# Kernel tuning notes

Hardware: AMD Instinct MI355X
Metric: run time of the kernel (lower is better)

The kernel has to match this reference:

```python
import jax, jax.numpy as jnp
import numpy as np

B, S, D, H, F = 2, 2048, 3072, 32, 8192
DH = D // H  # 96
EPS = 1e-5


def setup_inputs() -> dict:
    key = jax.random.key(0)
    ks = jax.random.split(key, 16)
    sd = 0.02
    inp = {
        "hidden_states": jax.random.normal(ks[0], (B, S, D), jnp.float32),
        "ln1_g": jnp.ones((D,), jnp.float32),
        "ln1_b": jnp.zeros((D,), jnp.float32),
        "Wq": jax.random.normal(ks[1], (D, H, DH), jnp.float32) * sd,
        "bq": jnp.zeros((H, DH), jnp.float32),
        "Wk": jax.random.normal(ks[2], (D, H, DH), jnp.float32) * sd,
        "bk": jnp.zeros((H, DH), jnp.float32),
        "Wv": jax.random.normal(ks[3], (D, H, DH), jnp.float32) * sd,
        "bv": jnp.zeros((H, DH), jnp.float32),
        "Wo": jax.random.normal(ks[4], (H, DH, D), jnp.float32) * sd,
        "bo": jnp.zeros((D,), jnp.float32),
        "ln2_g": jnp.ones((D,), jnp.float32),
        "ln2_b": jnp.zeros((D,), jnp.float32),
        "W1": jax.random.normal(ks[5], (D, F), jnp.float32) * sd,
        "b1": jnp.zeros((F,), jnp.float32),
        "W2": jax.random.normal(ks[6], (F, D), jnp.float32) * sd,
        "b2": jnp.zeros((D,), jnp.float32),
    }
    return inp


def _layernorm(x, g, b):
    m = jnp.mean(x, axis=-1, keepdims=True)
    v = jnp.mean(jnp.square(x - m), axis=-1, keepdims=True)
    return (x - m) * jax.lax.rsqrt(v + EPS) * g + b


def reference(hidden_states, ln1_g, ln1_b, Wq, bq, Wk, bk, Wv, bv, Wo, bo,
              ln2_g, ln2_b, W1, b1, W2, b2):
    # --- LN + self-attention + residual ---
    h = _layernorm(hidden_states, ln1_g, ln1_b)  # [B,S,D]
    q = jnp.einsum('bsd,dhk->bshk', h, Wq) + bq  # [B,S,H,DH]
    k = jnp.einsum('bsd,dhk->bshk', h, Wk) + bk
    v = jnp.einsum('bsd,dhk->bshk', h, Wv) + bv
    scale = 1.0 / np.sqrt(DH).astype(np.float32)
    scores = jnp.einsum('bshk,bthk->bhst', q, k) * scale  # [B,H,S,S]
    attn = jax.nn.softmax(scores, axis=-1)
    ctx = jnp.einsum('bhst,bthk->bshk', attn, v)  # [B,S,H,DH]
    attn_out = jnp.einsum('bshk,hkd->bsd', ctx, Wo) + bo
    h1 = hidden_states + attn_out
    # --- LN + MLP + residual ---
    h2 = _layernorm(h1, ln2_g, ln2_b)
    mlp = jax.nn.gelu(h2 @ W1 + b1, approximate=False) @ W2 + b2
    return h1 + mlp
```

## Files before the change

### kernel.cpp

```cpp
#include <hip/hip_runtime.h>
#include <math.h>

#define DEV __device__ __forceinline__

typedef __attribute__((ext_vector_type(8))) __bf16 bfrag;
typedef __attribute__((ext_vector_type(4))) float f4;
typedef __attribute__((ext_vector_type(8))) unsigned short u16x8;
typedef __attribute__((ext_vector_type(4))) unsigned short u16x4;

DEV unsigned short f2bf(float f) {
  unsigned u = __float_as_uint(f);
  u += 0x7fff + ((u >> 16) & 1);
  return (unsigned short)(u >> 16);
}

DEV void gload_lds16(const void* g, void* l) {
  __builtin_amdgcn_global_load_lds((const __attribute__((address_space(1))) void*)g,
                                   (__attribute__((address_space(3))) void*)l, 16, 0, 0);
}

template<int EPI, int OUTBF, int BIASROW>
__global__ __launch_bounds__(256, 2)
void gemm_bt(const unsigned short* __restrict__ A,
             const unsigned short* __restrict__ Bt,
             const float* __restrict__ bias,
             const float* __restrict__ res,
             void* __restrict__ outp,
             int M, int N, int K, int gm, int cm, int cn)
{
  __shared__ unsigned short As[2][128 * 32];
  __shared__ unsigned short Bs[2][128 * 32];
  const int tid = threadIdx.x;
  const int lane = tid & 63;
  const int wid = tid >> 6;
  const int wr = wid >> 1, wc = wid & 1;
  const int l15 = lane & 15, lg = lane >> 4;

  const int xcd = blockIdx.x & 7, bidx = blockIdx.x >> 3;
  const int cgm = gm / cm;
  const int tm = (xcd % cgm) * cm + bidx % cm;
  const int tn = (xcd / cgm) * cn + bidx / cm;
  const long tM = (long)tm * 128;
  const long tN = (long)tn * 128;

  const int c0 = tid, c1 = tid + 256;
  const int r0 = c0 >> 2, k0 = (c0 & 3) * 8;
  const int r1 = c1 >> 2, k1 = (c1 & 3) * 8;

  const unsigned short* A0 = A + (tM + r0) * (long)K + k0;
  const unsigned short* A1 = A + (tM + r1) * (long)K + k1;
  const unsigned short* B0 = Bt + (tN + r0) * (long)K + k0;
  const unsigned short* B1 = Bt + (tN + r1) * (long)K + k1;

  auto stage = [&](int kt, int buf) {
    const long ko = (long)kt * 32;
    gload_lds16(A0 + ko, &As[buf][c0 * 8]);
    gload_lds16(A1 + ko, &As[buf][c1 * 8]);
    gload_lds16(B0 + ko, &Bs[buf][c0 * 8]);
    gload_lds16(B1 + ko, &Bs[buf][c1 * 8]);
  };

  stage(0, 0);
  f4 acc[4][4] = {};
  const int nk = K >> 5;
  int cur = 0;
  __syncthreads();
  for (int kt = 0; kt < nk; ++kt) {
    if (kt + 1 < nk) stage(kt + 1, cur ^ 1);
    bfrag aF[4], bF[4];
#pragma unroll
    for (int m = 0; m < 4; ++m)
      aF[m] = *(const bfrag*)&As[cur][(wr * 64 + m * 16 + l15) * 32 + lg * 8];
#pragma unroll
    for (int n = 0; n < 4; ++n)
      bF[n] = *(const bfrag*)&Bs[cur][(wc * 64 + n * 16 + l15) * 32 + lg * 8];
#pragma unroll
    for (int m = 0; m < 4; ++m)
#pragma unroll
      for (int n = 0; n < 4; ++n)
        acc[m][n] = __builtin_amdgcn_mfma_f32_16x16x32_bf16(aF[m], bF[n], acc[m][n], 0, 0, 0);
    __syncthreads();
    cur ^= 1;
  }

#pragma unroll
  for (int m = 0; m < 4; ++m) {
#pragma unroll
    for (int n = 0; n < 4; ++n) {
      const long col = tN + wc * 64 + n * 16 + l15;
      const float bcol = BIASROW ? 0.f : bias[col];
#pragma unroll
      for (int e = 0; e < 4; ++e) {
        const long row = tM + wr * 64 + m * 16 + lg * 4 + e;
        float v = acc[m][n][e] + (BIASROW ? bias[row] : bcol);
        if constexpr (EPI == 1) v = 0.5f * v * (1.0f + erff(v * 0.70710678118654752f));
        if constexpr (EPI == 2) v += res[row * N + col];
        if constexpr (OUTBF) ((unsigned short*)outp)[row * N + col] = f2bf(v);
        else                 ((float*)outp)[row * N + col] = v;
      }
    }
  }
}

template<int EPI, int OUTBF, int BIASROW>
__global__ __launch_bounds__(512, 2)
void gemm256(const unsigned short* __restrict__ A,
             const unsigned short* __restrict__ Bt,
             const float* __restrict__ bias,
             const float* __restrict__ res,
             void* __restrict__ outp,
             int M, int N, int K, int gm, int cm, int cn)
{
  __shared__ unsigned short As[2][256 * 64];
  __shared__ unsigned short Bs[2][256 * 64];

  const int tid = threadIdx.x;
  const int lane = tid & 63;
  const int wid = tid >> 6;
  const int wm = wid >> 2, wn = wid & 3;
  const int l15 = lane & 15, lg = lane >> 4;

  const int xcd = blockIdx.x & 7, bidx = blockIdx.x >> 3;
  const int cgm = gm / cm;
  const int tm = (xcd % cgm) * cm + bidx % cm;
  const int tn = (xcd / cgm) * cn + bidx / cm;
  const long tM = (long)tm * 256, tN = (long)tn * 256;

  const int srow = tid >> 3;
  const int lslot = (tid & 7) ^ (srow & 7);
  const unsigned short* aSrc = A + (tM + srow) * (long)K + lslot * 8;
  const unsigned short* bSrc = Bt + (tN + srow) * (long)K + lslot * 8;
  const int NT = K >> 6;

  auto stA = [&](int t, int j) {
    gload_lds16(aSrc + (long)t * 64 + (long)j * 64 * K, &As[t & 1][j * 4096 + tid * 8]);
  };
  auto stB = [&](int t, int j) {
    gload_lds16(bSrc + (long)t * 64 + (long)j * 64 * K, &Bs[t & 1][j * 4096 + tid * 8]);
  };

#pragma unroll
  for (int j = 0; j < 4; ++j) stA(0, j);
#pragma unroll
  for (int j = 0; j < 4; ++j) stB(0, j);
  stA(1, 0); stA(1, 2);
#pragma unroll
  for (int j = 0; j < 4; ++j) stB(1, j);
  asm volatile("s_waitcnt vmcnt(6)" ::: "memory");
  __builtin_amdgcn_s_barrier();

  const int aRow = (wm * 128 + l15) * 64;
  const int bRow = (wn * 64 + l15) * 64;
  const int sx = l15 & 7;
  const int sl0 = ((0 + lg) ^ sx) * 8;
  const int sl1 = ((4 + lg) ^ sx) * 8;

  bfrag aL[4][2], aH[4][2], b01[2][2], b23[2][2];
  f4 acc[8][4] = {};

  int cur = 0;
  for (int t = 0; t < NT; ++t, cur ^= 1) {
    const unsigned short* Ac = As[cur];
    const unsigned short* Bc = Bs[cur];
    const bool s1 = (t + 1 < NT);
    const bool s2 = (t + 2 < NT);

#pragma unroll
    for (int m = 0; m < 4; ++m) {
      aL[m][0] = *(const bfrag*)&Ac[aRow + m * 1024 + sl0];
      aL[m][1] = *(const bfrag*)&Ac[aRow + m * 1024 + sl1];
    }
#pragma unroll
    for (int n = 0; n < 2; ++n) {
      b01[n][0] = *(const bfrag*)&Bc[bRow + n * 1024 + sl0];
      b01[n][1] = *(const bfrag*)&Bc[bRow + n * 1024 + sl1];
    }
#pragma unroll
    for (int n = 0; n < 2; ++n) {
      b23[n][0] = *(const bfrag*)&Bc[bRow + (n + 2) * 1024 + sl0];
      b23[n][1] = *(const bfrag*)&Bc[bRow + (n + 2) * 1024 + sl1];
    }
    if (s1) { stA(t + 1, 1); stA(t + 1, 3); }
    __builtin_amdgcn_s_barrier();
    __builtin_amdgcn_s_setprio(1);
#pragma unroll
    for (int m = 0; m < 4; ++m)
#pragma unroll
      for (int n = 0; n < 2; ++n) {
        acc[m][n] = __builtin_amdgcn_mfma_f32_16x16x32_bf16(aL[m][0], b01[n][0], acc[m][n], 0, 0, 0);
        acc[m][n] = __builtin_amdgcn_mfma_f32_16x16x32_bf16(aL[m][1], b01[n][1], acc[m][n], 0, 0, 0);
      }
    __builtin_amdgcn_s_setprio(0);
    __builtin_amdgcn_s_barrier();

#pragma unroll
    for (int m = 0; m < 4; ++m) {
      aH[m][0] = *(const bfrag*)&Ac[aRow + 4096 + m * 1024 + sl0];
      aH[m][1] = *(const bfrag*)&Ac[aRow + 4096 + m * 1024 + sl1];
    }
    if (s2) { stA(t + 2, 0); stA(t + 2, 2); }
    __builtin_amdgcn_s_barrier();
    __builtin_amdgcn_s_setprio(1);
#pragma unroll
    for (int m = 0; m < 4; ++m)
#pragma unroll
      for (int n = 0; n < 2; ++n) {
        acc[m][2 + n] = __builtin_amdgcn_mfma_f32_16x16x32_bf16(aL[m][0], b23[n][0], acc[m][2 + n], 0, 0, 0);
        acc[m][2 + n] = __builtin_amdgcn_mfma_f32_16x16x32_bf16(aL[m][1], b23[n][1], acc[m][2 + n], 0, 0, 0);
      }
    __builtin_amdgcn_s_setprio(0);
    __builtin_amdgcn_s_barrier();

    if (s2) { stB(t + 2, 0); stB(t + 2, 1); }
    __builtin_amdgcn_s_barrier();
    __builtin_amdgcn_s_setprio(1);
#pragma unroll
    for (int m = 0; m < 4; ++m)
#pragma unroll
      for (int n = 0; n < 2; ++n) {
        acc[4 + m][2 + n] = __builtin_amdgcn_mfma_f32_16x16x32_bf16(aH[m][0], b23[n][0], acc[4 + m][2 + n], 0, 0, 0);
        acc[4 + m][2 + n] = __builtin_amdgcn_mfma_f32_16x16x32_bf16(aH[m][1], b23[n][1], acc[4 + m][2 + n], 0, 0, 0);
      }
    __builtin_amdgcn_s_setprio(0);
    __builtin_amdgcn_s_barrier();

    if (s2) { stB(t + 2, 2); stB(t + 2, 3); }
    __builtin_amdgcn_s_setprio(1);
#pragma unroll
    for (int m = 0; m < 4; ++m)
#pragma unroll
      for (int n = 0; n < 2; ++n) {
        acc[4 + m][n] = __builtin_amdgcn_mfma_f32_16x16x32_bf16(aH[m][0], b01[n][0], acc[4 + m][n], 0, 0, 0);
        acc[4 + m][n] = __builtin_amdgcn_mfma_f32_16x16x32_bf16(aH[m][1], b01[n][1], acc[4 + m][n], 0, 0, 0);
      }
    __builtin_amdgcn_s_setprio(0);
    if (s2)      asm volatile("s_waitcnt vmcnt(6)" ::: "memory");
    else if (s1) asm volatile("s_waitcnt vmcnt(0)" ::: "memory");
    __builtin_amdgcn_s_barrier();
  }

#pragma unroll
  for (int m = 0; m < 8; ++m) {
    const long row0 = tM + wm * 128 + m * 16 + lg * 4;
#pragma unroll
    for (int n = 0; n < 4; ++n) {
      const long col = tN + wn * 64 + n * 16 + l15;
      const float bc = BIASROW ? 0.f : bias[col];
#pragma unroll
      for (int e = 0; e < 4; ++e) {
        const long row = row0 + e;
        float v = acc[m][n][e] + (BIASROW ? bias[row] : bc);
        if constexpr (EPI == 1) v = 0.5f * v * (1.0f + erff(v * 0.70710678118654752f));
        if constexpr (EPI == 2) v += res[row * N + col];
        if constexpr (OUTBF) ((unsigned short*)outp)[row * N + col] = f2bf(v);
        else                 ((float*)outp)[row * N + col] = v;
      }
    }
  }
}

__global__ __launch_bounds__(256)
void ln_bf16(const float* __restrict__ x, const float* __restrict__ g,
             const float* __restrict__ b, unsigned short* __restrict__ out)
{
  __shared__ float red[4];
  const int tid = threadIdx.x;
  const long row = blockIdx.x;
  const float* xr = x + row * 3072;
  float4 v[3];
  float s = 0.f;
#pragma unroll
  for (int i = 0; i < 3; ++i) {
    v[i] = *(const float4*)&xr[i * 1024 + tid * 4];
    s += v[i].x + v[i].y + v[i].z + v[i].w;
  }
#pragma unroll
  for (int o = 32; o > 0; o >>= 1) s += __shfl_xor(s, o);
  if ((tid & 63) == 0) red[tid >> 6] = s;
  __syncthreads();
  s = red[0] + red[1] + red[2] + red[3];
  const float mean = s * (1.f / 3072.f);
  float vs = 0.f;
#pragma unroll
  for (int i = 0; i < 3; ++i) {
    const float dx = v[i].x - mean, dy = v[i].y - mean;
    const float dz = v[i].z - mean, dw = v[i].w - mean;
    vs += dx * dx + dy * dy + dz * dz + dw * dw;
  }
#pragma unroll
  for (int o = 32; o > 0; o >>= 1) vs += __shfl_xor(vs, o);
  __syncthreads();
  if ((tid & 63) == 0) red[tid >> 6] = vs;
  __syncthreads();
  vs = red[0] + red[1] + red[2] + red[3];
  const float rstd = rsqrtf(vs * (1.f / 3072.f) + 1e-5f);
#pragma unroll
  for (int i = 0; i < 3; ++i) {
    const int idx = i * 1024 + tid * 4;
    const float* vp = (const float*)&v[i];
    u16x4 o4;
#pragma unroll
    for (int c = 0; c < 4; ++c)
      o4[c] = f2bf((vp[c] - mean) * rstd * g[idx + c] + b[idx + c]);
    *(u16x4*)&out[row * 3072 + idx] = o4;
  }
}

__global__ __launch_bounds__(256)
void prep_weights(const float* __restrict__ Wq, const float* __restrict__ Wk,
                  const float* __restrict__ Wv, const float* __restrict__ Wo,
                  const float* __restrict__ W1, const float* __restrict__ W2,
                  const float* __restrict__ bq, const float* __restrict__ bk,
                  unsigned short* __restrict__ WqkT, unsigned short* __restrict__ WvT,
                  unsigned short* __restrict__ WoT, unsigned short* __restrict__ W1T,
                  unsigned short* __restrict__ W2T, float* __restrict__ bqk)
{
  __shared__ float tile[32][33];
  int bid = blockIdx.x;
  if (bid < 24) {
    const int i = bid * 256 + threadIdx.x;
    bqk[i] = (i < 3072) ? bq[i] : bk[i - 3072];
    return;
  }
  bid -= 24;
  const float* in; unsigned short* out; int R, C, nbx;
  if (bid < 9216)        { in = Wq; out = WqkT;                R = 3072; C = 3072; nbx = 96; }
  else if (bid < 18432)  { in = Wk; out = WqkT + 3072 * 3072;  R = 3072; C = 3072; nbx = 96; bid -= 9216; }
  else if (bid < 27648)  { in = Wv; out = WvT;                 R = 3072; C = 3072; nbx = 96; bid -= 18432; }
  else if (bid < 36864)  { in = Wo; out = WoT;                 R = 3072; C = 3072; nbx = 96; bid -= 27648; }
  else if (bid < 61440)  { in = W1; out = W1T;                 R = 3072; C = 8192; nbx = 256; bid -= 36864; }
  else                   { in = W2; out = W2T;                 R = 8192; C = 3072; nbx = 96; bid -= 61440; }
  const int bx = bid % nbx, by = bid / nbx;
  const int tx = threadIdx.x & 31, ty = threadIdx.x >> 5;
  const long r0 = (long)by * 32, cc0 = (long)bx * 32;
#pragma unroll
  for (int i = 0; i < 4; ++i)
    tile[ty + 8 * i][tx] = in[(r0 + ty + 8 * i) * C + cc0 + tx];
  __syncthreads();
#pragma unroll
  for (int i = 0; i < 4; ++i)
    out[(cc0 + ty + 8 * i) * R + r0 + tx] = f2bf(tile[tx][ty + 8 * i]);
}

__global__ __launch_bounds__(256, 4)
void attn_fwd(const unsigned short* __restrict__ qk,
              const unsigned short* __restrict__ vT,
              unsigned short* __restrict__ ctx)
{
  __shared__ unsigned short Ks[64 * 104];
  __shared__ unsigned short Vt[96 * 72];
  __shared__ unsigned short Ps[4 * 16 * 72];
  const int tid = threadIdx.x;
  const int lane = tid & 63;
  const int w = tid >> 6;
  const int l15 = lane & 15, lg = lane >> 4;
  const int bid = (blockIdx.x & 7) * 256 + (blockIdx.x >> 3);
  const int qb = bid & 31;
  const int h = (bid >> 5) & 31;
  const int b = bid >> 10;
  const long qkbase = ((long)b * 2048) * 6144 + h * 96;
  const long obase  = ((long)b * 2048) * 3072 + h * 96;
  const long vbase  = (long)(h * 96) * 4096 + (long)b * 2048;
  const int qbase = qb * 64;

  bfrag qf[3];
#pragma unroll
  for (int ks = 0; ks < 3; ++ks)
    qf[ks] = *(const bfrag*)&qk[qkbase + (long)(qbase + w * 16 + l15) * 6144 + ks * 32 + lg * 8];

  const int kr0 = tid / 12,         kk0 = (tid % 12) * 8;
  const int kr1 = (tid + 256) / 12, kk1 = ((tid + 256) % 12) * 8;
  const int kr2 = (tid + 512) / 12, kk2 = ((tid + 512) % 12) * 8;
  const unsigned short* kg = qk + qkbase + 3072;
  const int vd0 = tid >> 3,           vk0 = (tid & 7) * 8;
  const int vd1 = (tid + 256) >> 3,   vk1 = ((tid + 256) & 7) * 8;
  const int vd2 = (tid + 512) >> 3,   vk2 = ((tid + 512) & 7) * 8;
  const unsigned short* vg = vT + vbase;

  u16x8 kA = *(const u16x8*)&kg[(long)kr0 * 6144 + kk0];
  u16x8 kB = *(const u16x8*)&kg[(long)kr1 * 6144 + kk1];
  u16x8 kC = *(const u16x8*)&kg[(long)kr2 * 6144 + kk2];
  u16x8 vA = *(const u16x8*)&vg[(long)vd0 * 4096 + vk0];
  u16x8 vB = *(const u16x8*)&vg[(long)vd1 * 4096 + vk1];
  u16x8 vC = *(const u16x8*)&vg[(long)vd2 * 4096 + vk2];

  float m_run = -1e30f, l_run = 0.f;
  f4 O[6] = {};
  const float sc = 0.1020620726f * 1.4426950409f;

  for (int t = 0; t < 32; ++t) {
    *(u16x8*)&Ks[kr0 * 104 + kk0] = kA;
    *(u16x8*)&Ks[kr1 * 104 + kk1] = kB;
    *(u16x8*)&Ks[kr2 * 104 + kk2] = kC;
    *(u16x8*)&Vt[vd0 * 72 + vk0] = vA;
    *(u16x8*)&Vt[vd1 * 72 + vk1] = vB;
    *(u16x8*)&Vt[vd2 * 72 + vk2] = vC;
    __syncthreads();
    if (t + 1 < 32) {
      const long ko = (long)(t + 1) * 64 * 6144;
      const long vo = (long)(t + 1) * 64;
      kA = *(const u16x8*)&kg[ko + (long)kr0 * 6144 + kk0];
      kB = *(const u16x8*)&kg[ko + (long)kr1 * 6144 + kk1];
      kC = *(const u16x8*)&kg[ko + (long)kr2 * 6144 + kk2];
      vA = *(const u16x8*)&vg[vo + (long)vd0 * 4096 + vk0];
      vB = *(const u16x8*)&vg[vo + (long)vd1 * 4096 + vk1];
      vC = *(const u16x8*)&vg[vo + (long)vd2 * 4096 + vk2];
    }

    f4 sf[4];
#pragma unroll
    for (int mb = 0; mb < 4; ++mb) {
      f4 z = {0.f, 0.f, 0.f, 0.f};
      sf[mb] = z;
#pragma unroll
      for (int ks = 0; ks < 3; ++ks) {
        bfrag kf = *(const bfrag*)&Ks[(mb * 16 + l15) * 104 + ks * 32 + lg * 8];
        sf[mb] = __builtin_amdgcn_mfma_f32_16x16x32_bf16(kf, qf[ks], sf[mb], 0, 0, 0);
      }
    }
    float p[16];
    float tmax = -1e30f;
#pragma unroll
    for (int mb = 0; mb < 4; ++mb)
#pragma unroll
      for (int e = 0; e < 4; ++e) {
        const float sv = sf[mb][e] * sc;
        p[mb * 4 + e] = sv;
        tmax = fmaxf(tmax, sv);
      }
    tmax = fmaxf(tmax, __shfl_xor(tmax, 16));
    tmax = fmaxf(tmax, __shfl_xor(tmax, 32));
    const float mnew = fmaxf(m_run, tmax);
    const float alpha = exp2f(m_run - mnew);
    float psum = 0.f;
#pragma unroll
    for (int i = 0; i < 16; ++i) {
      p[i] = exp2f(p[i] - mnew);
      psum += p[i];
    }
    psum += __shfl_xor(psum, 16);
    psum += __shfl_xor(psum, 32);
    l_run = l_run * alpha + psum;
    m_run = mnew;
#pragma unroll
    for (int mb = 0; mb < 4; ++mb) {
      u16x4 pw;
#pragma unroll
      for (int e = 0; e < 4; ++e) pw[e] = f2bf(p[mb * 4 + e]);
      *(u16x4*)&Ps[w * 1152 + l15 * 72 + mb * 16 + lg * 4] = pw;
    }
    float aE[4];
#pragma unroll
    for (int e = 0; e < 4; ++e) aE[e] = __shfl(alpha, lg * 4 + e);
#pragma unroll
    for (int nb = 0; nb < 6; ++nb)
#pragma unroll
      for (int e = 0; e < 4; ++e) O[nb][e] *= aE[e];
    bfrag pf[2];
#pragma unroll
    for (int ks = 0; ks < 2; ++ks)
      pf[ks] = *(const bfrag*)&Ps[w * 1152 + l15 * 72 + ks * 32 + lg * 8];
#pragma unroll
    for (int nb = 0; nb < 6; ++nb)
#pragma unroll
      for (int ks = 0; ks < 2; ++ks) {
        bfrag vf = *(const bfrag*)&Vt[(nb * 16 + l15) * 72 + ks * 32 + lg * 8];
        O[nb] = __builtin_amdgcn_mfma_f32_16x16x32_bf16(pf[ks], vf, O[nb], 0, 0, 0);
      }
    __syncthreads();
  }
  float lE[4];
#pragma unroll
  for (int e = 0; e < 4; ++e) lE[e] = 1.f / __shfl(l_run, lg * 4 + e);
#pragma unroll
  for (int nb = 0; nb < 6; ++nb)
#pragma unroll
    for (int e = 0; e < 4; ++e) {
      const long row = qbase + w * 16 + lg * 4 + e;
      ctx[obase + row * 3072 + nb * 16 + l15] = f2bf(O[nb][e] * lE[e]);
    }
}

extern "C" void kernel_launch(void* const* d_in, const int* in_sizes, int n_in,
                              void* d_out, int out_size, void* d_ws, size_t ws_size,
                              hipStream_t stream)
{
  (void)in_sizes; (void)n_in; (void)out_size; (void)ws_size;
  const float* x    = (const float*)d_in[0];
  const float* ln1g = (const float*)d_in[1];
  const float* ln1b = (const float*)d_in[2];
  const float* Wq   = (const float*)d_in[3];
  const float* bq   = (const float*)d_in[4];
  const float* Wk   = (const float*)d_in[5];
  const float* bk   = (const float*)d_in[6];
  const float* Wv   = (const float*)d_in[7];
  const float* bv   = (const float*)d_in[8];
  const float* Wo   = (const float*)d_in[9];
  const float* bo   = (const float*)d_in[10];
  const float* ln2g = (const float*)d_in[11];
  const float* ln2b = (const float*)d_in[12];
  const float* W1   = (const float*)d_in[13];
  const float* b1   = (const float*)d_in[14];
  const float* W2   = (const float*)d_in[15];
  const float* b2   = (const float*)d_in[16];

  char* ws = (char*)d_ws;
  unsigned short* WqkT = (unsigned short*)(ws + 0);
  unsigned short* WvT  = (unsigned short*)(ws + 37748736);
  unsigned short* WoT  = (unsigned short*)(ws + 56623104);
  unsigned short* W1T  = (unsigned short*)(ws + 75497472);
  unsigned short* W2T  = (unsigned short*)(ws + 125829120);
  float*          bqk  = (float*)(ws + 176160768);
  unsigned short* hbf  = (unsigned short*)(ws + 176185344);
  unsigned short* ctxb = hbf;
  unsigned short* qkb  = (unsigned short*)(ws + 201351168);
  unsigned short* h2   = qkb;
  unsigned short* act  = (unsigned short*)(ws + 251682816);
  unsigned short* vTb  = (unsigned short*)(ws + 318791680);
  float*          h1   = (float*)d_out;

  const dim3 blk(256);
  const dim3 blk512(512);

  prep_weights<<<24 + 86016, blk, 0, stream>>>(Wq, Wk, Wv, Wo, W1, W2, bq, bk,
                                               WqkT, WvT, WoT, W1T, W2T, bqk);

  ln_bf16<<<4096, blk, 0, stream>>>(x, ln1g, ln1b, hbf);

  gemm256<0, 1, 0><<<384, blk512, 0, stream>>>(hbf, WqkT, bqk, nullptr, qkb, 4096, 6144, 3072, 16, 8, 6);
  gemm256<0, 1, 1><<<192, blk512, 0, stream>>>(WvT, hbf, bv, nullptr, vTb, 3072, 4096, 3072, 12, 6, 4);

  attn_fwd<<<2048, blk, 0, stream>>>(qkb, vTb, ctxb);

  gemm256<2, 0, 0><<<192, blk512, 0, stream>>>(ctxb, WoT, bo, x, h1, 4096, 3072, 3072, 16, 4, 6);

  ln_bf16<<<4096, blk, 0, stream>>>(h1, ln2g, ln2b, h2);

  gemm256<1, 1, 0><<<512, blk512, 0, stream>>>(h2, W1T, b1, nullptr, act, 4096, 8192, 3072, 16, 8, 8);
  gemm_bt<2, 0, 0><<<768, blk, 0, stream>>>(act, W2T, b2, h1, (float*)d_out, 4096, 3072, 8192, 32, 16, 6);
}
```

Measured before the change: 1.192 ms.

## Process two 64-row query tiles per attention block to reuse K/V tiles

Each attention workgroup now handles 128 query rows, as two independent 64-row halves with separate online-softmax state, instead of 64. Every K/V tile staged in LDS therefore feeds twice as many MFMAs, which halves global K/V traffic and LDS fill work per query. The grid halves to 1024 blocks and launch bounds drop to 3 waves per SIMD. The cost is more registers for a second Q fragment set and accumulator, plus a second P buffer in LDS, which may reduce occupancy.

```diff
diff --git a/kernel.cpp b/kernel.cpp
--- a/kernel.cpp
+++ b/kernel.cpp
@@ -342,31 +342,33 @@
     out[(cc0 + ty + 8 * i) * R + r0 + tx] = f2bf(tile[tx][ty + 8 * i]);
 }
 
-__global__ __launch_bounds__(256, 4)
+__global__ __launch_bounds__(256, 3)
 void attn_fwd(const unsigned short* __restrict__ qk,
               const unsigned short* __restrict__ vT,
               unsigned short* __restrict__ ctx)
 {
   __shared__ unsigned short Ks[64 * 104];
   __shared__ unsigned short Vt[96 * 72];
-  __shared__ unsigned short Ps[4 * 16 * 72];
+  __shared__ unsigned short Ps[2][4 * 16 * 72];
   const int tid = threadIdx.x;
   const int lane = tid & 63;
   const int w = tid >> 6;
   const int l15 = lane & 15, lg = lane >> 4;
-  const int bid = (blockIdx.x & 7) * 256 + (blockIdx.x >> 3);
-  const int qb = bid & 31;
-  const int h = (bid >> 5) & 31;
-  const int b = bid >> 10;
+  const int bid = (blockIdx.x & 7) * 128 + (blockIdx.x >> 3);
+  const int qb = bid & 15;
+  const int h = (bid >> 4) & 31;
+  const int b = bid >> 9;
   const long qkbase = ((long)b * 2048) * 6144 + h * 96;
   const long obase  = ((long)b * 2048) * 3072 + h * 96;
   const long vbase  = (long)(h * 96) * 4096 + (long)b * 2048;
-  const int qbase = qb * 64;
-
-  bfrag qf[3];
-#pragma unroll
-  for (int ks = 0; ks < 3; ++ks)
-    qf[ks] = *(const bfrag*)&qk[qkbase + (long)(qbase + w * 16 + l15) * 6144 + ks * 32 + lg * 8];
+  const int qbase = qb * 128;
+
+  bfrag qf0[3], qf1[3];
+#pragma unroll
+  for (int ks = 0; ks < 3; ++ks) {
+    qf0[ks] = *(const bfrag*)&qk[qkbase + (long)(qbase + w * 16 + l15) * 6144 + ks * 32 + lg * 8];
+    qf1[ks] = *(const bfrag*)&qk[qkbase + (long)(qbase + 64 + w * 16 + l15) * 6144 + ks * 32 + lg * 8];
+  }
 
   const int kr0 = tid / 12,         kk0 = (tid % 12) * 8;
   const int kr1 = (tid + 256) / 12, kk1 = ((tid + 256) % 12) * 8;
@@ -384,8 +386,8 @@
   u16x8 vB = *(const u16x8*)&vg[(long)vd1 * 4096 + vk1];
   u16x8 vC = *(const u16x8*)&vg[(long)vd2 * 4096 + vk2];
 
-  float m_run = -1e30f, l_run = 0.f;
-  f4 O[6] = {};
+  float m0 = -1e30f, l0 = 0.f, m1 = -1e30f, l1 = 0.f;
+  f4 O0[6] = {}, O1[6] = {};
   const float sc = 0.1020620726f * 1.4426950409f;
 
   for (int t = 0; t < 32; ++t) {
@@ -407,77 +409,130 @@
       vC = *(const u16x8*)&vg[vo + (long)vd2 * 4096 + vk2];
     }
 
-    f4 sf[4];
+    f4 sf0[4], sf1[4];
 #pragma unroll
     for (int mb = 0; mb < 4; ++mb) {
       f4 z = {0.f, 0.f, 0.f, 0.f};
-      sf[mb] = z;
+      sf0[mb] = z; sf1[mb] = z;
 #pragma unroll
       for (int ks = 0; ks < 3; ++ks) {
         bfrag kf = *(const bfrag*)&Ks[(mb * 16 + l15) * 104 + ks * 32 + lg * 8];
-        sf[mb] = __builtin_amdgcn_mfma_f32_16x16x32_bf16(kf, qf[ks], sf[mb], 0, 0, 0);
-      }
-    }
-    float p[16];
-    float tmax = -1e30f;
-#pragma unroll
-    for (int mb = 0; mb < 4; ++mb)
-#pragma unroll
-      for (int e = 0; e < 4; ++e) {
-        const float sv = sf[mb][e] * sc;
-        p[mb * 4 + e] = sv;
-        tmax = fmaxf(tmax, sv);
-      }
-    tmax = fmaxf(tmax, __shfl_xor(tmax, 16));
-    tmax = fmaxf(tmax, __shfl_xor(tmax, 32));
-    const float mnew = fmaxf(m_run, tmax);
-    const float alpha = exp2f(m_run - mnew);
-    float psum = 0.f;
-#pragma unroll
-    for (int i = 0; i < 16; ++i) {
-      p[i] = exp2f(p[i] - mnew);
-      psum += p[i];
-    }
-    psum += __shfl_xor(psum, 16);
-    psum += __shfl_xor(psum, 32);
-    l_run = l_run * alpha + psum;
-    m_run = mnew;
-#pragma unroll
-    for (int mb = 0; mb < 4; ++mb) {
-      u16x4 pw;
-#pragma unroll
-      for (int e = 0; e < 4; ++e) pw[e] = f2bf(p[mb * 4 + e]);
-      *(u16x4*)&Ps[w * 1152 + l15 * 72 + mb * 16 + lg * 4] = pw;
-    }
-    float aE[4];
-#pragma unroll
-    for (int e = 0; e < 4; ++e) aE[e] = __shfl(alpha, lg * 4 + e);
-#pragma unroll
-    for (int nb = 0; nb < 6; ++nb)
-#pragma unroll
-      for (int e = 0; e < 4; ++e) O[nb][e] *= aE[e];
-    bfrag pf[2];
-#pragma unroll
-    for (int ks = 0; ks < 2; ++ks)
-      pf[ks] = *(const bfrag*)&Ps[w * 1152 + l15 * 72 + ks * 32 + lg * 8];
+        sf0[mb] = __builtin_amdgcn_mfma_f32_16x16x32_bf16(kf, qf0[ks], sf0[mb], 0, 0, 0);
+        sf1[mb] = __builtin_amdgcn_mfma_f32_16x16x32_bf16(kf, qf1[ks], sf1[mb], 0, 0, 0);
+      }
+    }
+
+    {
+      float p[16];
+      float tmax = -1e30f;
+#pragma unroll
+      for (int mb = 0; mb < 4; ++mb)
+#pragma unroll
+        for (int e = 0; e < 4; ++e) {
+          const float sv = sf0[mb][e] * sc;
+          p[mb * 4 + e] = sv;
+          tmax = fmaxf(tmax, sv);
+        }
+      tmax = fmaxf(tmax, __shfl_xor(tmax, 16));
+      tmax = fmaxf(tmax, __shfl_xor(tmax, 32));
+      const float mnew = fmaxf(m0, tmax);
+      const float alpha = exp2f(m0 - mnew);
+      float psum = 0.f;
+#pragma unroll
+      for (int i = 0; i < 16; ++i) {
+        p[i] = exp2f(p[i] - mnew);
+        psum += p[i];
+      }
+      psum += __shfl_xor(psum, 16);
+      psum += __shfl_xor(psum, 32);
+      l0 = l0 * alpha + psum;
+      m0 = mnew;
+#pragma unroll
+      for (int mb = 0; mb < 4; ++mb) {
+        u16x4 pw;
+#pragma unroll
+        for (int e = 0; e < 4; ++e) pw[e] = f2bf(p[mb * 4 + e]);
+        *(u16x4*)&Ps[0][w * 1152 + l15 * 72 + mb * 16 + lg * 4] = pw;
+      }
+      float aE[4];
+#pragma unroll
+      for (int e = 0; e < 4; ++e) aE[e] = __shfl(alpha, lg * 4 + e);
+#pragma unroll
+      for (int nb = 0; nb < 6; ++nb)
+#pragma unroll
+        for (int e = 0; e < 4; ++e) O0[nb][e] *= aE[e];
+    }
+    {
+      float p[16];
+      float tmax = -1e30f;
+#pragma unroll
+      for (int mb = 0; mb < 4; ++mb)
+#pragma unroll
+        for (int e = 0; e < 4; ++e) {
+          const float sv = sf1[mb][e] * sc;
+          p[mb * 4 + e] = sv;
+          tmax = fmaxf(tmax, sv);
+        }
+      tmax = fmaxf(tmax, __shfl_xor(tmax, 16));
+      tmax = fmaxf(tmax, __shfl_xor(tmax, 32));
+      const float mnew = fmaxf(m1, tmax);
+      const float alpha = exp2f(m1 - mnew);
+      float psum = 0.f;
+#pragma unroll
+      for (int i = 0; i < 16; ++i) {
+        p[i] = exp2f(p[i] - mnew);
+        psum += p[i];
+      }
+      psum += __shfl_xor(psum, 16);
+      psum += __shfl_xor(psum, 32);
+      l1 = l1 * alpha + psum;
+      m1 = mnew;
+#pragma unroll
+      for (int mb = 0; mb < 4; ++mb) {
+        u16x4 pw;
+#pragma unroll
+        for (int e = 0; e < 4; ++e) pw[e] = f2bf(p[mb * 4 + e]);
+        *(u16x4*)&Ps[1][w * 1152 + l15 * 72 + mb * 16 + lg * 4] = pw;
+      }
+      float aE[4];
+#pragma unroll
+      for (int e = 0; e < 4; ++e) aE[e] = __shfl(alpha, lg * 4 + e);
+#pragma unroll
+      for (int nb = 0; nb < 6; ++nb)
+#pragma unroll
+        for (int e = 0; e < 4; ++e) O1[nb][e] *= aE[e];
+    }
+
+    bfrag pf0[2], pf1[2];
+#pragma unroll
+    for (int ks = 0; ks < 2; ++ks) {
+      pf0[ks] = *(const bfrag*)&Ps[0][w * 1152 + l15 * 72 + ks * 32 + lg * 8];
+      pf1[ks] = *(const bfrag*)&Ps[1][w * 1152 + l15 * 72 + ks * 32 + lg * 8];
+    }
 #pragma unroll
     for (int nb = 0; nb < 6; ++nb)
 #pragma unroll
       for (int ks = 0; ks < 2; ++ks) {
         bfrag vf = *(const bfrag*)&Vt[(nb * 16 + l15) * 72 + ks * 32 + lg * 8];
-        O[nb] = __builtin_amdgcn_mfma_f32_16x16x32_bf16(pf[ks], vf, O[nb], 0, 0, 0);
+        O0[nb] = __builtin_amdgcn_mfma_f32_16x16x32_bf16(pf0[ks], vf, O0[nb], 0, 0, 0);
+        O1[nb] = __builtin_amdgcn_mfma_f32_16x16x32_bf16(pf1[ks], vf, O1[nb], 0, 0, 0);
       }
     __syncthreads();
   }
-  float lE[4];
-#pragma unroll
-  for (int e = 0; e < 4; ++e) lE[e] = 1.f / __shfl(l_run, lg * 4 + e);
+
+  float lE0[4], lE1[4];
+#pragma unroll
+  for (int e = 0; e < 4; ++e) {
+    lE0[e] = 1.f / __shfl(l0, lg * 4 + e);
+    lE1[e] = 1.f / __shfl(l1, lg * 4 + e);
+  }
 #pragma unroll
   for (int nb = 0; nb < 6; ++nb)
 #pragma unroll
     for (int e = 0; e < 4; ++e) {
-      const long row = qbase + w * 16 + lg * 4 + e;
-      ctx[obase + row * 3072 + nb * 16 + l15] = f2bf(O[nb][e] * lE[e]);
+      const long row0 = qbase + w * 16 + lg * 4 + e;
+      ctx[obase + row0 * 3072 + nb * 16 + l15] = f2bf(O0[nb][e] * lE0[e]);
+      ctx[obase + (row0 + 64) * 3072 + nb * 16 + l15] = f2bf(O1[nb][e] * lE1[e]);
     }
 }
 
@@ -530,7 +585,7 @@
   gemm256<0, 1, 0><<<384, blk512, 0, stream>>>(hbf, WqkT, bqk, nullptr, qkb, 4096, 6144, 3072, 16, 8, 6);
   gemm256<0, 1, 1><<<192, blk512, 0, stream>>>(WvT, hbf, bv, nullptr, vTb, 3072, 4096, 3072, 12, 6, 4);
 
-  attn_fwd<<<2048, blk, 0, stream>>>(qkb, vTb, ctxb);
+  attn_fwd<<<1024, blk, 0, stream>>>(qkb, vTb, ctxb);
 
   gemm256<2, 0, 0><<<192, blk512, 0, stream>>>(ctxb, WoT, bo, x, h1, 4096, 3072, 3072, 16, 4, 6);
 
```

Result: slower. 1.252 ms (+5.0%).
